# Kernel tuning notes

Measured on AMD Instinct MI355X. Metric: run time of the kernel, lower is better.

The kernel has to match this reference:

```python
import jax, jax.numpy as jnp
import numpy as np

N_NODES = 20000
N_EDGES = 320000
F_DIM = 64      # num_features == hidden_units
HID = 64
N_RUNS = 10
N_GRAPHS = 128
N_CLASSES = 10
N_LAYERS = 4
BN_EPS = 1e-5
P_DROP = 0.2


def _batchnorm(t, g, b):
    # training-mode BatchNorm1d over the flattened (num_runs*N, d) rows, biased variance
    mu = jnp.mean(t, axis=0)
    var = jnp.mean(jnp.square(t - mu), axis=0)
    return (t - mu) * jax.lax.rsqrt(var + BN_EPS) * g + b


def setup_inputs() -> dict:
    key = jax.random.key(0)
    ks = jax.random.split(key, 16)
    x = jax.random.normal(ks[0], (N_NODES, F_DIM), jnp.float32)
    edge_index = jax.random.randint(ks[1], (2, N_EDGES), 0, N_NODES, dtype=jnp.int32)
    batch = jnp.sort(jax.random.randint(ks[2], (N_NODES,), 0, N_GRAPHS, dtype=jnp.int32))
    drop_mask = jax.random.uniform(ks[3], (N_RUNS, N_NODES)) < P_DROP
    s = 0.1
    conv_w1 = jax.random.normal(ks[4], (N_LAYERS, F_DIM, HID), jnp.float32) * s
    conv_b1 = jax.random.normal(ks[5], (N_LAYERS, HID), jnp.float32) * s
    bn1_g = jax.random.uniform(ks[6], (N_LAYERS, HID), jnp.float32, 0.5, 1.5)
    bn1_b = jax.random.normal(ks[7], (N_LAYERS, HID), jnp.float32) * s
    conv_w2 = jax.random.normal(ks[8], (N_LAYERS, HID, HID), jnp.float32) * s
    conv_b2 = jax.random.normal(ks[9], (N_LAYERS, HID), jnp.float32) * s
    bn_g = jax.random.uniform(ks[10], (N_LAYERS, HID), jnp.float32, 0.5, 1.5)
    bn_b = jax.random.normal(ks[11], (N_LAYERS, HID), jnp.float32) * s
    fc_w = jax.random.normal(ks[12], (N_LAYERS + 1, HID, N_CLASSES), jnp.float32) * s
    fc_b = jax.random.normal(ks[13], (N_LAYERS + 1, N_CLASSES), jnp.float32) * s
    return dict(x=x, edge_index=edge_index, batch=batch, drop_mask=drop_mask,
                conv_w1=conv_w1, conv_b1=conv_b1, bn1_g=bn1_g, bn1_b=bn1_b,
                conv_w2=conv_w2, conv_b2=conv_b2, bn_g=bn_g, bn_b=bn_b,
                fc_w=fc_w, fc_b=fc_b)


def reference(x, edge_index, batch, drop_mask,
              conv_w1, conv_b1, bn1_g, bn1_b, conv_w2, conv_b2, bn_g, bn_b,
              fc_w, fc_b):
    # prediction path (eval): node-drop, 4 GIN layers over num_runs replicated
    # graphs, per-level mean-over-runs + global_add_pool + fc, sum, log_softmax.
    R = drop_mask.shape[0]
    N = x.shape[0]
    src, dst = edge_index[0], edge_index[1]
    # replicated node features with stochastic node drop: [R, N, F]
    h = jnp.where(drop_mask[..., None], jnp.zeros((), x.dtype), x[None])
    outs = [h]
    for i in range(N_LAYERS):
        # GINConv (eps=0): MLP(x + sum_{j->i} x_j); vectorized over runs
        # (equivalent to the original offset-replicated run_edge_index).
        agg = jnp.zeros_like(h).at[:, dst].add(h[:, src])  # [R, N, d]
        z = (h + agg).reshape(R * N, -1)
        t = z @ conv_w1[i] + conv_b1[i]
        t = jax.nn.relu(_batchnorm(t, bn1_g[i], bn1_b[i]))
        t = t @ conv_w2[i] + conv_b2[i]
        t = jax.nn.relu(_batchnorm(t, bn_g[i], bn_b[i]))
        h = t.reshape(R, N, -1)
        outs.append(h)
    out = jnp.zeros((N_GRAPHS, N_CLASSES), x.dtype)
    for i, o in enumerate(outs):
        m = jnp.mean(o, axis=0)  # [N, d] mean over runs
        pooled = jax.ops.segment_sum(m, batch, num_segments=N_GRAPHS)  # global_add_pool
        out = out + pooled @ fc_w[i] + fc_b[i]  # dropout is identity in eval
    return jax.nn.log_softmax(out, axis=-1)
```

## Files before the change

### kernel.cpp

```cpp
#include <hip/hip_runtime.h>

#define N_NODES 20000
#define N_EDGES 320000
#define R_RUNS 10
#define HID 64
#define NG 128
#define NC 10
#define NL 4
#define MROWS (R_RUNS * N_NODES)
#define BN_EPS 1e-5f
#define NCOPY 16
#define TS 72

typedef __bf16 bf16;
typedef __attribute__((ext_vector_type(8))) __bf16 bf16x8;
typedef __attribute__((ext_vector_type(4))) float f32x4;
typedef unsigned int uint32;

constexpr size_t OFF_FLAGS   = 0;
constexpr size_t OFF_CURSOR  = 256;
constexpr size_t OFF_STATS   = 80640;
constexpr size_t OFF_POOLED5 = 146176;
constexpr size_t ZERO_BYTES  = 310016;
constexpr size_t OFF_ROWST   = 310016;
constexpr size_t OFF_COL     = 390400;
constexpr size_t OFF_PARAMS  = 1670400;
constexpr size_t OFF_XB      = 1745664;
constexpr size_t OFF_H       = 4305664;
constexpr size_t OFF_Z       = 29905664;

#define PW1  0
#define PB1  16384
#define PG1  16640
#define PBB1 16896
#define PW2  17152
#define PB2  33536
#define PG2  33792
#define PBB2 34048
#define PFW  34304
#define PFB  37504
#define PTOT 37554
#define CVT_TOT (1280000 + PTOT)

__global__ void detect_kernel(const unsigned short* __restrict__ xu,
                              const unsigned int* __restrict__ mw,
                              int* __restrict__ cnts) {
    int tid = blockIdx.x * 256 + threadIdx.x;
    int insane = 0, lowp = 0, f32w = 0, gt1 = 0;
    for (int i = tid; i < 4096; i += 16384) {
        unsigned int u = xu[2 * i];
        if (((u >> 7) & 0xFFu) >= 0x90u) insane++;
    }
    for (int i = tid; i < 50000; i += 16384) {
        unsigned int w = mw[i];
        if ((w & 0xFFFFu) == 0x3F80u) lowp = 1;
        else if (w == 0x3F800000u) f32w = 1;
        else if (w > 1u) gt1 = 1;
    }
    if (insane) atomicAdd(&cnts[0], insane);
    if (lowp)   atomicOr(&cnts[1], 1);
    if (f32w)   atomicOr(&cnts[2], 1);
    if (gt1)    atomicOr(&cnts[3], 1);
}

__device__ inline bf16 ld_any(const void* p, int i, int f32mode) {
    if (f32mode) return (bf16)((const float*)p)[i];
    return ((const bf16*)p)[i];
}

__global__ void convert_kernel(const int* __restrict__ cnts,
                               const void* x, const void* w1, const void* b1,
                               const void* g1, const void* bb1, const void* w2,
                               const void* b2, const void* g2, const void* bb2,
                               const void* fw, const void* fb,
                               bf16* __restrict__ xb, bf16* __restrict__ params) {
    int t = blockIdx.x * 256 + threadIdx.x;
    if (t >= CVT_TOT) return;
    int f = cnts[0] > 64;
    if (t < 1280000) { xb[t] = ld_any(x, t, f); return; }
    int u = t - 1280000;
    if (u < PB1 || (u >= PW2 && u < PB2)) {
        const void* src = (u < PB1) ? w1 : w2;
        int v = (u < PB1) ? u : u - PW2;
        int layer = v >> 12, rem = v & 4095;
        int j = rem & 7, lane = (rem >> 3) & 63, ntc = rem >> 9;
        int nt = ntc >> 1, c = ntc & 1;
        int k = c * 32 + (lane >> 4) * 8 + j;
        int n = nt * 16 + (lane & 15);
        params[u] = ld_any(src, layer * 4096 + k * 64 + n, f);
        return;
    }
    const void* src; int base;
    if      (u < PG1)  { src = b1;  base = PB1; }
    else if (u < PBB1) { src = g1;  base = PG1; }
    else if (u < PW2)  { src = bb1; base = PBB1; }
    else if (u < PG2)  { src = b2;  base = PB2; }
    else if (u < PBB2) { src = g2;  base = PG2; }
    else if (u < PFW)  { src = bb2; base = PBB2; }
    else if (u < PFB)  { src = fw;  base = PFW; }
    else               { src = fb;  base = PFB; }
    params[u] = ld_any(src, u - base, f);
}

__global__ void build_h0_pool_kernel(const bf16* __restrict__ xb,
                                     const void* __restrict__ maskp,
                                     const int* __restrict__ cnts,
                                     const int* __restrict__ batch,
                                     bf16* __restrict__ h,
                                     float* __restrict__ pooled) {
    int t = blockIdx.x * 256 + threadIdx.x;
    int c = t & 7, n = t >> 3;
    int w = cnts[1] ? 2 : (cnts[2] ? 4 : (cnts[3] ? 1 : 4));
    bf16x8 xv = *(const bf16x8*)(xb + (size_t)n * HID + c * 8);
    bf16x8 zv;
    #pragma unroll
    for (int j = 0; j < 8; ++j) zv[j] = (bf16)0.0f;
    float s[8];
    #pragma unroll
    for (int j = 0; j < 8; ++j) s[j] = 0.f;
    #pragma unroll
    for (int r = 0; r < R_RUNS; ++r) {
        size_t midx = (size_t)r * N_NODES + n;
        int dropped;
        if (w == 1)      dropped = ((const unsigned char*)maskp)[midx] != 0;
        else if (w == 2) dropped = ((const unsigned short*)maskp)[midx] != 0;
        else             dropped = ((const unsigned int*)maskp)[midx] != 0;
        *(bf16x8*)(h + ((size_t)n * R_RUNS + r) * HID + c * 8) = dropped ? zv : xv;
        if (!dropped)
            #pragma unroll
            for (int j = 0; j < 8; ++j) s[j] += (float)xv[j];
    }
    int g = batch[n];
    #pragma unroll
    for (int j = 0; j < 8; ++j)
        atomicAdd(&pooled[g * HID + c * 8 + j], s[j] * (1.0f / R_RUNS));
}

__global__ void csr_count_kernel(const int* __restrict__ ei, int* __restrict__ deg) {
    int e = blockIdx.x * 256 + threadIdx.x;
    if (e < N_EDGES) atomicAdd(&deg[ei[N_EDGES + e]], 1);
}

__global__ void csr_scan_kernel(int* __restrict__ deg, int* __restrict__ row_start) {
    __shared__ int lds[1024];
    int tid = threadIdx.x;
    const int CH = 20;
    int base = tid * CH;
    int local[CH];
    int s = 0;
    #pragma unroll
    for (int j = 0; j < CH; ++j) {
        int n = base + j;
        int d = (n < N_NODES) ? deg[n] : 0;
        local[j] = d; s += d;
    }
    lds[tid] = s; __syncthreads();
    for (int off = 1; off < 1024; off <<= 1) {
        int add = (tid >= off) ? lds[tid - off] : 0;
        __syncthreads();
        lds[tid] += add;
        __syncthreads();
    }
    int excl = lds[tid] - s;
    #pragma unroll
    for (int j = 0; j < CH; ++j) {
        int n = base + j;
        if (n < N_NODES) { row_start[n] = excl; deg[n] = excl; excl += local[j]; }
    }
    if (tid == 1023) row_start[N_NODES] = lds[1023];
}

__global__ void csr_fill_kernel(const int* __restrict__ ei, int* __restrict__ cursor,
                                int* __restrict__ col) {
    int e = blockIdx.x * 256 + threadIdx.x;
    if (e < N_EDGES) {
        int src = ei[e];
        int dst = ei[N_EDGES + e];
        int pos = atomicAdd(&cursor[dst], 1);
        col[pos] = src;
    }
}

__global__ __launch_bounds__(256) void ag1_kernel(const uint32* __restrict__ hD,
                                                  const int* __restrict__ row_start,
                                                  const int* __restrict__ col,
                                                  const bf16* __restrict__ Wf,
                                                  const bf16* __restrict__ bias,
                                                  bf16* __restrict__ out,
                                                  float* __restrict__ statsOut) {
    __shared__ __align__(16) bf16 zT[16 * R_RUNS * TS];
    __shared__ float lsum[64], lsq[64];
    uint32* zTu = (uint32*)zT;
    int tid = threadIdx.x;
    int wave = tid >> 6, lane = tid & 63, l16 = lane & 15, quad = lane >> 4;
    int b = blockIdx.x;
    const int NODE_DW = R_RUNS * HID / 2;

    if (tid < 64) { lsum[tid] = 0.f; lsq[tid] = 0.f; }

    for (int i = 0; i < 4; ++i) {
        int nl = wave + 4 * i;
        int n = b * 16 + nl;
        size_t base4 = (size_t)n * NODE_DW + lane * 4;
        size_t baset = (size_t)n * NODE_DW + 256 + lane;
        float acc[10];
        {
            uint4 u = *(const uint4*)(hD + base4);
            uint32 tw = hD[baset];
            acc[0] = __uint_as_float(u.x << 16); acc[1] = __uint_as_float(u.x & 0xFFFF0000u);
            acc[2] = __uint_as_float(u.y << 16); acc[3] = __uint_as_float(u.y & 0xFFFF0000u);
            acc[4] = __uint_as_float(u.z << 16); acc[5] = __uint_as_float(u.z & 0xFFFF0000u);
            acc[6] = __uint_as_float(u.w << 16); acc[7] = __uint_as_float(u.w & 0xFFFF0000u);
            acc[8] = __uint_as_float(tw << 16);  acc[9] = __uint_as_float(tw & 0xFFFF0000u);
        }
        int beg = row_start[n], end = row_start[n + 1];
        int idx = beg;
        for (; idx + 4 <= end; idx += 4) {
            uint4 a[4]; uint32 tw[4];
            #pragma unroll
            for (int u = 0; u < 4; ++u) {
                size_t o = (size_t)col[idx + u] * NODE_DW;
                a[u] = *(const uint4*)(hD + o + lane * 4);
                tw[u] = hD[o + 256 + lane];
            }
            #pragma unroll
            for (int u = 0; u < 4; ++u) {
                uint32 wd[4] = {a[u].x, a[u].y, a[u].z, a[u].w};
                #pragma unroll
                for (int c = 0; c < 4; ++c) {
                    acc[2 * c]     += __uint_as_float(wd[c] << 16);
                    acc[2 * c + 1] += __uint_as_float(wd[c] & 0xFFFF0000u);
                }
                acc[8] += __uint_as_float(tw[u] << 16);
                acc[9] += __uint_as_float(tw[u] & 0xFFFF0000u);
            }
        }
        for (; idx < end; ++idx) {
            size_t o = (size_t)col[idx] * NODE_DW;
            uint4 a0 = *(const uint4*)(hD + o + lane * 4);
            uint32 t0 = hD[o + 256 + lane];
            uint32 wd[4] = {a0.x, a0.y, a0.z, a0.w};
            #pragma unroll
            for (int c = 0; c < 4; ++c) {
                acc[2 * c]     += __uint_as_float(wd[c] << 16);
                acc[2 * c + 1] += __uint_as_float(wd[c] & 0xFFFF0000u);
            }
            acc[8] += __uint_as_float(t0 << 16);
            acc[9] += __uint_as_float(t0 & 0xFFFF0000u);
        }
        #pragma unroll
        for (int c = 0; c < 5; ++c) {
            int d = (c < 4) ? (lane * 4 + c) : (256 + lane);
            int rL = nl * R_RUNS + (d >> 5);
            int fp = d & 31;
            unsigned short lo = __builtin_bit_cast(unsigned short, (bf16)acc[2 * c]);
            unsigned short hi = __builtin_bit_cast(unsigned short, (bf16)acc[2 * c + 1]);
            zTu[rL * (TS / 2) + fp] = (uint32)lo | ((uint32)hi << 16);
        }
    }
    __syncthreads();

    bf16x8 bfr[4][2];
    #pragma unroll
    for (int nt = 0; nt < 4; ++nt)
        #pragma unroll
        for (int c = 0; c < 2; ++c)
            bfr[nt][c] = *(const bf16x8*)(Wf + (size_t)((nt * 2 + c) * 64 + lane) * 8);
    float bvs[4];
    #pragma unroll
    for (int nt = 0; nt < 4; ++nt) bvs[nt] = (float)bias[nt * 16 + l16];

    for (int g = wave; g < 10; g += 4) {
        const bf16* tp = &zT[(g * 16 + l16) * TS];
        bf16x8 a0 = *(const bf16x8*)(tp + quad * 8);
        bf16x8 a1 = *(const bf16x8*)(tp + 32 + quad * 8);
        f32x4 acc[4];
        #pragma unroll
        for (int nt = 0; nt < 4; ++nt) acc[nt] = (f32x4){bvs[nt], bvs[nt], bvs[nt], bvs[nt]};
        #pragma unroll
        for (int nt = 0; nt < 4; ++nt) {
            acc[nt] = __builtin_amdgcn_mfma_f32_16x16x32_bf16(a0, bfr[nt][0], acc[nt], 0, 0, 0);
            acc[nt] = __builtin_amdgcn_mfma_f32_16x16x32_bf16(a1, bfr[nt][1], acc[nt], 0, 0, 0);
        }
        size_t rowBase = (size_t)b * 160 + g * 16;
        #pragma unroll
        for (int nt = 0; nt < 4; ++nt) {
            float ss = 0.f, qq = 0.f;
            #pragma unroll
            for (int reg = 0; reg < 4; ++reg) {
                float v = acc[nt][reg];
                ss += v; qq += v * v;
                out[(rowBase + quad * 4 + reg) * HID + nt * 16 + l16] = (bf16)v;
            }
            atomicAdd(&lsum[nt * 16 + l16], ss);
            atomicAdd(&lsq[nt * 16 + l16], qq);
        }
    }
    __syncthreads();
    if (tid < 64) {
        int copy = b & (NCOPY - 1);
        atomicAdd(&statsOut[copy * 128 + tid], lsum[tid]);
        atomicAdd(&statsOut[copy * 128 + 64 + tid], lsq[tid]);
    }
}

__global__ __launch_bounds__(256) void gemm64_kernel(const bf16* in,
                                                     const bf16* __restrict__ Wf,
                                                     const bf16* __restrict__ bias,
                                                     bf16* out,
                                                     const float* __restrict__ statsIn,
                                                     const bf16* __restrict__ gammaIn,
                                                     const bf16* __restrict__ betaIn,
                                                     float* __restrict__ statsOut) {
    __shared__ float lstat[128];
    __shared__ float lscale[64], lshift[64];
    __shared__ float lsum[64], lsq[64];
    int tid = threadIdx.x;
    int wave = tid >> 6, lane = tid & 63, l16 = lane & 15, quad = lane >> 4;

    if (tid < 128) {
        float s = 0.f;
        #pragma unroll
        for (int k = 0; k < NCOPY; ++k) s += statsIn[k * 128 + tid];
        lstat[tid] = s;
    }
    if (tid < 64) { lsum[tid] = 0.f; lsq[tid] = 0.f; }
    __syncthreads();
    if (tid < 64) {
        float mu = lstat[tid] * (1.0f / MROWS);
        float var = lstat[tid + 64] * (1.0f / MROWS) - mu * mu;
        float rs = rsqrtf(var + BN_EPS);
        float a = (float)gammaIn[tid] * rs;
        lscale[tid] = a;
        lshift[tid] = (float)betaIn[tid] - mu * a;
    }
    __syncthreads();

    size_t rowBase = (size_t)blockIdx.x * 64 + wave * 16;

    bf16x8 bfrag[4][2];
    #pragma unroll
    for (int nt = 0; nt < 4; ++nt)
        #pragma unroll
        for (int c = 0; c < 2; ++c)
            bfrag[nt][c] = *(const bf16x8*)(Wf + (size_t)((nt * 2 + c) * 64 + lane) * 8);

    f32x4 acc[4];
    #pragma unroll
    for (int nt = 0; nt < 4; ++nt) {
        float bv = (float)bias[nt * 16 + l16];
        acc[nt] = (f32x4){bv, bv, bv, bv};
    }

    size_t row = rowBase + l16;
    bf16x8 afrag[2];
    #pragma unroll
    for (int c = 0; c < 2; ++c) {
        int k0 = c * 32 + quad * 8;
        bf16x8 v = *(const bf16x8*)(in + row * HID + k0);
        #pragma unroll
        for (int j = 0; j < 8; ++j) {
            float f = (float)v[j] * lscale[k0 + j] + lshift[k0 + j];
            v[j] = (bf16)fmaxf(f, 0.f);
        }
        afrag[c] = v;
    }

    #pragma unroll
    for (int nt = 0; nt < 4; ++nt) {
        acc[nt] = __builtin_amdgcn_mfma_f32_16x16x32_bf16(afrag[0], bfrag[nt][0], acc[nt], 0, 0, 0);
        acc[nt] = __builtin_amdgcn_mfma_f32_16x16x32_bf16(afrag[1], bfrag[nt][1], acc[nt], 0, 0, 0);
    }

    #pragma unroll
    for (int nt = 0; nt < 4; ++nt)
        #pragma unroll
        for (int reg = 0; reg < 4; ++reg) {
            size_t orow = rowBase + quad * 4 + reg;
            out[orow * HID + nt * 16 + l16] = (bf16)acc[nt][reg];
        }

    #pragma unroll
    for (int nt = 0; nt < 4; ++nt) {
        float s = 0.f, q = 0.f;
        #pragma unroll
        for (int reg = 0; reg < 4; ++reg) { float v = acc[nt][reg]; s += v; q += v * v; }
        atomicAdd(&lsum[nt * 16 + l16], s);
        atomicAdd(&lsq[nt * 16 + l16], q);
    }
    __syncthreads();
    if (tid < 64) {
        int copy = blockIdx.x & (NCOPY - 1);
        atomicAdd(&statsOut[copy * 128 + tid], lsum[tid]);
        atomicAdd(&statsOut[copy * 128 + 64 + tid], lsq[tid]);
    }
}

__global__ __launch_bounds__(256) void pool_bn_kernel(const bf16* __restrict__ t,
                                                      const float* __restrict__ statsIn,
                                                      const bf16* __restrict__ gammaIn,
                                                      const bf16* __restrict__ betaIn,
                                                      bf16* __restrict__ hOut,
                                                      const int* __restrict__ batch,
                                                      float* __restrict__ pooled) {
    __shared__ float lstat[128], lscale[64], lshift[64];
    int tid = threadIdx.x;
    if (tid < 128) {
        float s = 0.f;
        #pragma unroll
        for (int k = 0; k < NCOPY; ++k) s += statsIn[k * 128 + tid];
        lstat[tid] = s;
    }
    __syncthreads();
    if (tid < 64) {
        float mu = lstat[tid] * (1.0f / MROWS);
        float var = lstat[tid + 64] * (1.0f / MROWS) - mu * mu;
        float rs = rsqrtf(var + BN_EPS);
        float a = (float)gammaIn[tid] * rs;
        lscale[tid] = a;
        lshift[tid] = (float)betaIn[tid] - mu * a;
    }
    __syncthreads();
    int gid = blockIdx.x * 256 + tid;
    int f = tid & 63, n = gid >> 6;
    float sc = lscale[f], sh = lshift[f];
    size_t base = (size_t)n * (R_RUNS * HID) + f;
    float s = 0.f;
    #pragma unroll
    for (int r = 0; r < R_RUNS; ++r) {
        float v = (float)t[base + r * HID];
        v = fmaxf(v * sc + sh, 0.f);
        hOut[base + r * HID] = (bf16)v;
        s += v;
    }
    atomicAdd(&pooled[batch[n] * HID + f], s * (1.0f / R_RUNS));
}

__global__ void fc_softmax_kernel(const float* __restrict__ pooled5,
                                  const bf16* __restrict__ params,
                                  const int* __restrict__ cnts, void* __restrict__ out) {
    int g = threadIdx.x;
    if (g >= NG) return;
    float o[NC];
    #pragma unroll
    for (int c = 0; c < NC; ++c) o[c] = 0.f;
    for (int l = 0; l < NL + 1; ++l) {
        const float* pg = pooled5 + ((size_t)l * NG + g) * HID;
        const bf16* fw = params + PFW + l * (HID * NC);
        for (int k = 0; k < HID; ++k) {
            float p = pg[k];
            #pragma unroll
            for (int c = 0; c < NC; ++c) o[c] += p * (float)fw[k * NC + c];
        }
        #pragma unroll
        for (int c = 0; c < NC; ++c) o[c] += (float)params[PFB + l * NC + c];
    }
    float m = -1e30f;
    #pragma unroll
    for (int c = 0; c < NC; ++c) m = fmaxf(m, o[c]);
    float s = 0.f;
    #pragma unroll
    for (int c = 0; c < NC; ++c) s += expf(o[c] - m);
    float lg = logf(s);
    int f = cnts[0] > 64;
    #pragma unroll
    for (int c = 0; c < NC; ++c) {
        float val = o[c] - m - lg;
        if (f) ((float*)out)[g * NC + c] = val;
        else   ((bf16*)out)[g * NC + c] = (bf16)val;
    }
}

extern "C" void kernel_launch(void* const* d_in, const int* in_sizes, int n_in,
                              void* d_out, int out_size, void* d_ws, size_t ws_size,
                              hipStream_t stream) {
    const void* x     = d_in[0];
    const int*  ei    = (const int*)d_in[1];
    const int*  batch = (const int*)d_in[2];
    const void* maskp = d_in[3];

    char* ws = (char*)d_ws;
    int*   cnts    = (int*)(ws + OFF_FLAGS);
    int*   cursor  = (int*)(ws + OFF_CURSOR);
    float* statsb  = (float*)(ws + OFF_STATS);
    float* pooled5 = (float*)(ws + OFF_POOLED5);
    int*   rowst   = (int*)(ws + OFF_ROWST);
    int*   colbuf  = (int*)(ws + OFF_COL);
    bf16*  params  = (bf16*)(ws + OFF_PARAMS);
    bf16*  xb      = (bf16*)(ws + OFF_XB);
    bf16*  h       = (bf16*)(ws + OFF_H);
    bf16*  z       = (bf16*)(ws + OFF_Z);

    hipMemsetAsync(ws, 0, ZERO_BYTES, stream);

    detect_kernel<<<64, 256, 0, stream>>>((const unsigned short*)x,
                                          (const unsigned int*)maskp, cnts);
    convert_kernel<<<(CVT_TOT + 255) / 256, 256, 0, stream>>>(
        cnts, x, d_in[4], d_in[5], d_in[6], d_in[7], d_in[8], d_in[9], d_in[10],
        d_in[11], d_in[12], d_in[13], xb, params);

    csr_count_kernel<<<(N_EDGES + 255) / 256, 256, 0, stream>>>(ei, cursor);
    csr_scan_kernel<<<1, 1024, 0, stream>>>(cursor, rowst);
    csr_fill_kernel<<<(N_EDGES + 255) / 256, 256, 0, stream>>>(ei, cursor, colbuf);

    build_h0_pool_kernel<<<(N_NODES * 8) / 256, 256, 0, stream>>>(
        xb, maskp, cnts, batch, h, pooled5);

    for (int i = 0; i < NL; ++i) {
        float* st1 = statsb + (size_t)(2 * i) * (NCOPY * 128);
        float* st2 = statsb + (size_t)(2 * i + 1) * (NCOPY * 128);

        ag1_kernel<<<N_NODES / 16, 256, 0, stream>>>(
            (const uint32*)h, rowst, colbuf,
            params + PW1 + i * 4096, params + PB1 + i * 64, z, st1);

        gemm64_kernel<<<MROWS / 64, 256, 0, stream>>>(
            z, params + PW2 + i * 4096, params + PB2 + i * 64, z,
            st1, params + PG1 + i * 64, params + PBB1 + i * 64, st2);

        pool_bn_kernel<<<(N_NODES * HID) / 256, 256, 0, stream>>>(
            z, st2, params + PG2 + i * 64, params + PBB2 + i * 64, h, batch,
            pooled5 + (size_t)(i + 1) * NG * HID);
    }

    fc_softmax_kernel<<<1, 128, 0, stream>>>(pooled5, params, cnts, d_out);
}
```

Measured before the change: 887.0 us.

## Finalize BatchNorm stats in last block via ticket; split h0 build and pooling

```diff
diff --git a/kernel.cpp b/kernel.cpp
--- a/kernel.cpp
+++ b/kernel.cpp
@@ -18,16 +18,18 @@
 typedef unsigned int uint32;
 
 constexpr size_t OFF_FLAGS   = 0;
+constexpr size_t OFF_TICKETS = 64;
 constexpr size_t OFF_CURSOR  = 256;
 constexpr size_t OFF_STATS   = 80640;
 constexpr size_t OFF_POOLED5 = 146176;
 constexpr size_t ZERO_BYTES  = 310016;
-constexpr size_t OFF_ROWST   = 310016;
-constexpr size_t OFF_COL     = 390400;
-constexpr size_t OFF_PARAMS  = 1670400;
-constexpr size_t OFF_XB      = 1745664;
-constexpr size_t OFF_H       = 4305664;
-constexpr size_t OFF_Z       = 29905664;
+constexpr size_t OFF_SCSH    = 310016;
+constexpr size_t OFF_ROWST   = 311040;
+constexpr size_t OFF_COL     = 391424;
+constexpr size_t OFF_PARAMS  = 1671424;
+constexpr size_t OFF_XB      = 1746688;
+constexpr size_t OFF_H       = 4306688;
+constexpr size_t OFF_Z       = 29906688;
 
 #define PW1  0
 #define PB1  16384
@@ -102,38 +104,39 @@
     params[u] = ld_any(src, u - base, f);
 }
 
-__global__ void build_h0_pool_kernel(const bf16* __restrict__ xb,
-                                     const void* __restrict__ maskp,
-                                     const int* __restrict__ cnts,
-                                     const int* __restrict__ batch,
-                                     bf16* __restrict__ h,
-                                     float* __restrict__ pooled) {
-    int t = blockIdx.x * 256 + threadIdx.x;
-    int c = t & 7, n = t >> 3;
+__global__ void build_h0_kernel(const bf16* __restrict__ xb, const void* __restrict__ maskp,
+                                const int* __restrict__ cnts, bf16* __restrict__ h) {
+    int i = blockIdx.x * 256 + threadIdx.x;
+    int c = i & 7;
+    int rowid = i >> 3;
+    int r = rowid % R_RUNS;
+    int n = rowid / R_RUNS;
+    size_t midx = (size_t)r * N_NODES + n;
     int w = cnts[1] ? 2 : (cnts[2] ? 4 : (cnts[3] ? 1 : 4));
-    bf16x8 xv = *(const bf16x8*)(xb + (size_t)n * HID + c * 8);
-    bf16x8 zv;
-    #pragma unroll
-    for (int j = 0; j < 8; ++j) zv[j] = (bf16)0.0f;
-    float s[8];
-    #pragma unroll
-    for (int j = 0; j < 8; ++j) s[j] = 0.f;
-    #pragma unroll
-    for (int r = 0; r < R_RUNS; ++r) {
-        size_t midx = (size_t)r * N_NODES + n;
-        int dropped;
-        if (w == 1)      dropped = ((const unsigned char*)maskp)[midx] != 0;
-        else if (w == 2) dropped = ((const unsigned short*)maskp)[midx] != 0;
-        else             dropped = ((const unsigned int*)maskp)[midx] != 0;
-        *(bf16x8*)(h + ((size_t)n * R_RUNS + r) * HID + c * 8) = dropped ? zv : xv;
-        if (!dropped)
-            #pragma unroll
-            for (int j = 0; j < 8; ++j) s[j] += (float)xv[j];
-    }
-    int g = batch[n];
-    #pragma unroll
-    for (int j = 0; j < 8; ++j)
-        atomicAdd(&pooled[g * HID + c * 8 + j], s[j] * (1.0f / R_RUNS));
+    int dropped;
+    if (w == 1)      dropped = ((const unsigned char*)maskp)[midx] != 0;
+    else if (w == 2) dropped = ((const unsigned short*)maskp)[midx] != 0;
+    else             dropped = ((const unsigned int*)maskp)[midx] != 0;
+    bf16x8 v;
+    if (dropped) {
+        #pragma unroll
+        for (int j = 0; j < 8; ++j) v[j] = (bf16)0.0f;
+    } else {
+        v = *(const bf16x8*)(xb + (size_t)n * HID + c * 8);
+    }
+    *(bf16x8*)(h + (size_t)rowid * HID + c * 8) = v;
+}
+
+__global__ __launch_bounds__(256) void pool0_kernel(const bf16* __restrict__ t,
+                                                    const int* __restrict__ batch,
+                                                    float* __restrict__ pooled) {
+    int gid = blockIdx.x * 256 + threadIdx.x;
+    int f = gid & 63, n = gid >> 6;
+    size_t base = (size_t)n * (R_RUNS * HID) + f;
+    float s = 0.f;
+    #pragma unroll
+    for (int r = 0; r < R_RUNS; ++r) s += (float)t[base + r * HID];
+    atomicAdd(&pooled[batch[n] * HID + f], s * (1.0f / R_RUNS));
 }
 
 __global__ void csr_count_kernel(const int* __restrict__ ei, int* __restrict__ deg) {
@@ -181,15 +184,44 @@
     }
 }
 
+__device__ inline void finalize_stats(int tid, const float* statsP,
+                                      const bf16* gamma, const bf16* beta,
+                                      float* scaleOut, float* shiftOut,
+                                      float* lstat) {
+    if (tid < 128) {
+        float s = 0.f;
+        #pragma unroll
+        for (int k = 0; k < NCOPY; ++k)
+            s += __hip_atomic_load(&statsP[k * 128 + tid], __ATOMIC_RELAXED,
+                                   __HIP_MEMORY_SCOPE_AGENT);
+        lstat[tid] = s;
+    }
+    __syncthreads();
+    if (tid < 64) {
+        float mu = lstat[tid] * (1.0f / MROWS);
+        float var = lstat[tid + 64] * (1.0f / MROWS) - mu * mu;
+        float rs = rsqrtf(var + BN_EPS);
+        float a = (float)gamma[tid] * rs;
+        scaleOut[tid] = a;
+        shiftOut[tid] = (float)beta[tid] - mu * a;
+    }
+}
+
 __global__ __launch_bounds__(256) void ag1_kernel(const uint32* __restrict__ hD,
                                                   const int* __restrict__ row_start,
                                                   const int* __restrict__ col,
                                                   const bf16* __restrict__ Wf,
                                                   const bf16* __restrict__ bias,
                                                   bf16* __restrict__ out,
-                                                  float* __restrict__ statsOut) {
+                                                  float* __restrict__ statsOut,
+                                                  int* __restrict__ ticket,
+                                                  const bf16* __restrict__ gamma,
+                                                  const bf16* __restrict__ beta,
+                                                  float* __restrict__ scaleOut,
+                                                  float* __restrict__ shiftOut) {
     __shared__ __align__(16) bf16 zT[16 * R_RUNS * TS];
-    __shared__ float lsum[64], lsq[64];
+    __shared__ float lsum[64], lsq[64], lstat[128];
+    __shared__ int isLast;
     uint32* zTu = (uint32*)zT;
     int tid = threadIdx.x;
     int wave = tid >> 6, lane = tid & 63, l16 = lane & 15, quad = lane >> 4;
@@ -302,37 +334,39 @@
         atomicAdd(&statsOut[copy * 128 + tid], lsum[tid]);
         atomicAdd(&statsOut[copy * 128 + 64 + tid], lsq[tid]);
     }
+    if (tid == 0) {
+        __threadfence();
+        int old = __hip_atomic_fetch_add(ticket, 1, __ATOMIC_ACQ_REL,
+                                         __HIP_MEMORY_SCOPE_AGENT);
+        isLast = (old == (int)gridDim.x - 1);
+    }
+    __syncthreads();
+    if (isLast)
+        finalize_stats(tid, statsOut, gamma, beta, scaleOut, shiftOut, lstat);
 }
 
 __global__ __launch_bounds__(256) void gemm64_kernel(const bf16* in,
                                                      const bf16* __restrict__ Wf,
                                                      const bf16* __restrict__ bias,
                                                      bf16* out,
-                                                     const float* __restrict__ statsIn,
-                                                     const bf16* __restrict__ gammaIn,
-                                                     const bf16* __restrict__ betaIn,
-                                                     float* __restrict__ statsOut) {
-    __shared__ float lstat[128];
+                                                     const float* __restrict__ scaleIn,
+                                                     const float* __restrict__ shiftIn,
+                                                     float* __restrict__ statsOut,
+                                                     int* __restrict__ ticket,
+                                                     const bf16* __restrict__ gamma,
+                                                     const bf16* __restrict__ beta,
+                                                     float* __restrict__ scaleOut,
+                                                     float* __restrict__ shiftOut) {
     __shared__ float lscale[64], lshift[64];
-    __shared__ float lsum[64], lsq[64];
+    __shared__ float lsum[64], lsq[64], lstat[128];
+    __shared__ int isLast;
     int tid = threadIdx.x;
     int wave = tid >> 6, lane = tid & 63, l16 = lane & 15, quad = lane >> 4;
 
-    if (tid < 128) {
-        float s = 0.f;
-        #pragma unroll
-        for (int k = 0; k < NCOPY; ++k) s += statsIn[k * 128 + tid];
-        lstat[tid] = s;
-    }
-    if (tid < 64) { lsum[tid] = 0.f; lsq[tid] = 0.f; }
-    __syncthreads();
     if (tid < 64) {
-        float mu = lstat[tid] * (1.0f / MROWS);
-        float var = lstat[tid + 64] * (1.0f / MROWS) - mu * mu;
-        float rs = rsqrtf(var + BN_EPS);
-        float a = (float)gammaIn[tid] * rs;
-        lscale[tid] = a;
-        lshift[tid] = (float)betaIn[tid] - mu * a;
+        lscale[tid] = scaleIn[tid];
+        lshift[tid] = shiftIn[tid];
+        lsum[tid] = 0.f; lsq[tid] = 0.f;
     }
     __syncthreads();
 
@@ -394,36 +428,27 @@
         atomicAdd(&statsOut[copy * 128 + tid], lsum[tid]);
         atomicAdd(&statsOut[copy * 128 + 64 + tid], lsq[tid]);
     }
+    if (tid == 0) {
+        __threadfence();
+        int old = __hip_atomic_fetch_add(ticket, 1, __ATOMIC_ACQ_REL,
+                                         __HIP_MEMORY_SCOPE_AGENT);
+        isLast = (old == (int)gridDim.x - 1);
+    }
+    __syncthreads();
+    if (isLast)
+        finalize_stats(tid, statsOut, gamma, beta, scaleOut, shiftOut, lstat);
 }
 
 __global__ __launch_bounds__(256) void pool_bn_kernel(const bf16* __restrict__ t,
-                                                      const float* __restrict__ statsIn,
-                                                      const bf16* __restrict__ gammaIn,
-                                                      const bf16* __restrict__ betaIn,
+                                                      const float* __restrict__ scaleIn,
+                                                      const float* __restrict__ shiftIn,
                                                       bf16* __restrict__ hOut,
                                                       const int* __restrict__ batch,
                                                       float* __restrict__ pooled) {
-    __shared__ float lstat[128], lscale[64], lshift[64];
     int tid = threadIdx.x;
-    if (tid < 128) {
-        float s = 0.f;
-        #pragma unroll
-        for (int k = 0; k < NCOPY; ++k) s += statsIn[k * 128 + tid];
-        lstat[tid] = s;
-    }
-    __syncthreads();
-    if (tid < 64) {
-        float mu = lstat[tid] * (1.0f / MROWS);
-        float var = lstat[tid + 64] * (1.0f / MROWS) - mu * mu;
-        float rs = rsqrtf(var + BN_EPS);
-        float a = (float)gammaIn[tid] * rs;
-        lscale[tid] = a;
-        lshift[tid] = (float)betaIn[tid] - mu * a;
-    }
-    __syncthreads();
     int gid = blockIdx.x * 256 + tid;
     int f = tid & 63, n = gid >> 6;
-    float sc = lscale[f], sh = lshift[f];
+    float sc = scaleIn[f], sh = shiftIn[f];
     size_t base = (size_t)n * (R_RUNS * HID) + f;
     float s = 0.f;
     #pragma unroll
@@ -481,15 +506,18 @@
 
     char* ws = (char*)d_ws;
     int*   cnts    = (int*)(ws + OFF_FLAGS);
+    int*   tickets = (int*)(ws + OFF_TICKETS);
     int*   cursor  = (int*)(ws + OFF_CURSOR);
     float* statsb  = (float*)(ws + OFF_STATS);
     float* pooled5 = (float*)(ws + OFF_POOLED5);
+    float* scsh    = (float*)(ws + OFF_SCSH);
     int*   rowst   = (int*)(ws + OFF_ROWST);
     int*   colbuf  = (int*)(ws + OFF_COL);
     bf16*  params  = (bf16*)(ws + OFF_PARAMS);
     bf16*  xb      = (bf16*)(ws + OFF_XB);
     bf16*  h       = (bf16*)(ws + OFF_H);
     bf16*  z       = (bf16*)(ws + OFF_Z);
+    float* sc1 = scsh, *sh1 = scsh + 64, *sc2 = scsh + 128, *sh2 = scsh + 192;
 
     hipMemsetAsync(ws, 0, ZERO_BYTES, stream);
 
@@ -503,8 +531,8 @@
     csr_scan_kernel<<<1, 1024, 0, stream>>>(cursor, rowst);
     csr_fill_kernel<<<(N_EDGES + 255) / 256, 256, 0, stream>>>(ei, cursor, colbuf);
 
-    build_h0_pool_kernel<<<(N_NODES * 8) / 256, 256, 0, stream>>>(
-        xb, maskp, cnts, batch, h, pooled5);
+    build_h0_kernel<<<(MROWS * 8) / 256, 256, 0, stream>>>(xb, maskp, cnts, h);
+    pool0_kernel<<<(N_NODES * HID) / 256, 256, 0, stream>>>(h, batch, pooled5);
 
     for (int i = 0; i < NL; ++i) {
         float* st1 = statsb + (size_t)(2 * i) * (NCOPY * 128);
@@ -512,15 +540,16 @@
 
         ag1_kernel<<<N_NODES / 16, 256, 0, stream>>>(
             (const uint32*)h, rowst, colbuf,
-            params + PW1 + i * 4096, params + PB1 + i * 64, z, st1);
+            params + PW1 + i * 4096, params + PB1 + i * 64, z, st1,
+            &tickets[i], params + PG1 + i * 64, params + PBB1 + i * 64, sc1, sh1);
 
         gemm64_kernel<<<MROWS / 64, 256, 0, stream>>>(
             z, params + PW2 + i * 4096, params + PB2 + i * 64, z,
-            st1, params + PG1 + i * 64, params + PBB1 + i * 64, st2);
+            sc1, sh1, st2,
+            &tickets[4 + i], params + PG2 + i * 64, params + PBB2 + i * 64, sc2, sh2);
 
         pool_bn_kernel<<<(N_NODES * HID) / 256, 256, 0, stream>>>(
-            z, st2, params + PG2 + i * 64, params + PBB2 + i * 64, h, batch,
-            pooled5 + (size_t)(i + 1) * NG * HID);
+            z, sc2, sh2, h, batch, pooled5 + (size_t)(i + 1) * NG * HID);
     }
 
     fc_softmax_kernel<<<1, 128, 0, stream>>>(pooled5, params, cnts, d_out);
```

New measurement: 1.734 ms. 95.5% more time.
